# Optimization experiments

Hardware: AMD Instinct MI355X
Metric: run time of the kernel (lower is better)

## Reference

```python
import jax, jax.numpy as jnp
import numpy as np

HIDDEN = 2048
H = 16            # num heads
Q_RANK = 1536
KV_RANK = 512
D_NOPE = 128
D_ROPE = 64
D_QK = D_NOPE + D_ROPE   # 192
D_V = 128
ROPE_BASE = 10000.0
EPS = 1e-6


def _rms_norm(x, w):
    xf = x.astype(jnp.float32)
    var = jnp.mean(xf * xf, axis=-1, keepdims=True)
    return w * (xf * jax.lax.rsqrt(var + EPS)).astype(x.dtype)


def _rotate_half(x):
    x1, x2 = x[..., : x.shape[-1] // 2], x[..., x.shape[-1] // 2:]
    return jnp.concatenate((-x2, x1), axis=-1)


def _rope_cos_sin(position_ids, dtype):
    inv_freq = 1.0 / (ROPE_BASE ** (jnp.arange(0, D_ROPE, 2, dtype=jnp.float32) / D_ROPE))
    freqs = position_ids.astype(jnp.float32)[..., None] * inv_freq  # [b,s,32]
    emb = jnp.concatenate((freqs, freqs), axis=-1)                  # [b,s,64]
    return jnp.cos(emb).astype(dtype), jnp.sin(emb).astype(dtype)


def setup_inputs() -> dict:
    key = jax.random.key(0)
    ks = jax.random.split(key, 8)
    b, s = 1, 2048
    scale = 0.02
    return {
        "hidden_states": jax.random.normal(ks[0], (b, s, HIDDEN), jnp.float32),
        "position_ids": jnp.broadcast_to(jnp.arange(s, dtype=jnp.int64)[None, :], (b, s)),
        "q_a_w": jax.random.normal(ks[1], (Q_RANK, HIDDEN), jnp.float32) * scale,
        "q_a_ln_w": jnp.ones((Q_RANK,), jnp.float32),
        "q_b_w": jax.random.normal(ks[2], (H * D_QK, Q_RANK), jnp.float32) * scale,
        "kv_a_w": jax.random.normal(ks[3], (KV_RANK + D_ROPE, HIDDEN), jnp.float32) * scale,
        "kv_a_ln_w": jnp.ones((KV_RANK,), jnp.float32),
        "kv_b_w": jax.random.normal(ks[4], (H * (D_NOPE + D_V), KV_RANK), jnp.float32) * scale,
        "o_w": jax.random.normal(ks[5], (HIDDEN, H * D_V), jnp.float32) * scale,
    }


def reference(hidden_states, position_ids, q_a_w, q_a_ln_w, q_b_w, kv_a_w, kv_a_ln_w, kv_b_w, o_w):
    b, s, _ = hidden_states.shape
    softmax_scale = D_QK ** (-0.5)

    # Q path: low-rank down-proj -> RMSNorm -> up-proj
    q_a = hidden_states @ q_a_w.T                              # [b,s,q_rank]
    q = (_rms_norm(q_a, q_a_ln_w) @ q_b_w.T).reshape(b, s, H, D_QK)
    q_nope, q_pe = q[..., :D_NOPE], q[..., D_NOPE:]

    # KV path: joint down-proj -> split latent / rope part
    kv_a = hidden_states @ kv_a_w.T                            # [b,s,kv_rank+rope]
    compressed_kv = _rms_norm(kv_a[..., :KV_RANK], kv_a_ln_w)  # [b,s,kv_rank]
    k_pe = kv_a[..., KV_RANK:]                                 # [b,s,rope]
    kv_b = (compressed_kv @ kv_b_w.T).reshape(b, s, H, D_NOPE + D_V)
    k_nope, v = kv_b[..., :D_NOPE], kv_b[..., D_NOPE:]

    # decoupled RoPE on the rope slice
    cos, sin = _rope_cos_sin(position_ids, hidden_states.dtype)  # [b,s,64]
    cos, sin = cos[:, :, None, :], sin[:, :, None, :]            # [b,s,1,64]
    q_pe = q_pe * cos + _rotate_half(q_pe) * sin                 # [b,s,H,64]
    k_pe_h = jnp.broadcast_to(k_pe[:, :, None, :], (b, s, H, D_ROPE))
    k_pe_h = k_pe_h * cos + _rotate_half(k_pe_h) * sin

    q_full = jnp.concatenate([q_nope, q_pe], axis=-1)            # [b,s,H,192]
    k_full = jnp.concatenate([k_nope, k_pe_h], axis=-1)          # [b,s,H,192]

    # naive materialized attention (matches reference)
    scores = jnp.einsum("bqhd,bkhd->bhqk", q_full, k_full) * softmax_scale
    causal = jnp.triu(jnp.full((s, s), -jnp.inf, dtype=scores.dtype), k=1)
    scores = scores + causal
    probs = jax.nn.softmax(scores.astype(jnp.float32), axis=-1).astype(q_full.dtype)
    attn = jnp.einsum("bhqk,bkhd->bqhd", probs, v).reshape(b, s, H * D_V)
    return attn @ o_w.T
```

## Files before the change

kernel.cpp:

```cpp
#include <hip/hip_runtime.h>
#include <stdint.h>

#define S_LEN 2048
#define HIDDEN_ 2048
#define NH 16
#define QR 1536
#define KVR 512
#define DN 128
#define DR 64
#define DQK 192
#define DV 128
#define NQKV 2112

typedef __attribute__((ext_vector_type(8))) short bf16x8;
typedef __attribute__((ext_vector_type(4))) float f32x4;
typedef __attribute__((ext_vector_type(4))) unsigned short u16x4;
typedef unsigned short u16;
typedef unsigned int u32;

#define GLOAD_LDS16(g, l)                                                      \
    __builtin_amdgcn_global_load_lds(                                          \
        (const __attribute__((address_space(1))) void*)(g),                    \
        (__attribute__((address_space(3))) void*)(l), 16, 0, 0)

__device__ inline float bf2f(u16 x) {
    union { u32 u; float f; } v; v.u = ((u32)x) << 16; return v.f;
}
__device__ inline u16 f2bf(float f) {
    union { float f; u32 u; } v; v.f = f;
    u32 u = v.u;
    return (u16)((u + 0x7fffu + ((u >> 16) & 1u)) >> 16);
}

__global__ void cvt_multi(const float* s0, u16* d0, int n0,
                          const float* s1, u16* d1, int n1,
                          const float* s2, u16* d2, int n2,
                          const float* s3, u16* d3, int n3,
                          const float* s4, u16* d4, int n4,
                          const float* s5, u16* d5, int n5)
{
    const float* src; u16* dst; int n;
    switch (blockIdx.y) {
        case 0: src = s0; dst = d0; n = n0; break;
        case 1: src = s1; dst = d1; n = n1; break;
        case 2: src = s2; dst = d2; n = n2; break;
        case 3: src = s3; dst = d3; n = n3; break;
        case 4: src = s4; dst = d4; n = n4; break;
        default: src = s5; dst = d5; n = n5; break;
    }
    int i = (blockIdx.x * 256 + threadIdx.x) * 4;
    if (i + 3 < n) {
        float4 v = *(const float4*)(src + i);
        u16x4 o;
        o[0] = f2bf(v.x); o[1] = f2bf(v.y); o[2] = f2bf(v.z); o[3] = f2bf(v.w);
        *(u16x4*)(dst + i) = o;
    }
}

__device__ __forceinline__
void gemm_body(const u16* __restrict__ A, const u16* __restrict__ B,
               void* __restrict__ Cv, int M, int N, int Kloop, int ld,
               int out_f32, int bx, int by)
{
    __shared__ u16 sA[128 * 32];
    __shared__ u16 sB[128 * 32];
    const int tid  = threadIdx.x;
    const int wave = tid >> 6;
    const int lane = tid & 63;
    const int l16  = lane & 15;
    const int quad = lane >> 4;
    const int m_blk = by * 128;
    const int n_blk = bx * 128;
    const int wm = (wave >> 1) * 64;
    const int wn = (wave & 1) * 64;

    const f32x4 zero4 = {0.f, 0.f, 0.f, 0.f};
    f32x4 acc[4][4];
#pragma unroll
    for (int i = 0; i < 4; i++)
#pragma unroll
        for (int j = 0; j < 4; j++) acc[i][j] = zero4;

    const int srow = lane >> 2;
    const int scol = (lane & 3) * 8;

    for (int k0 = 0; k0 < Kloop; k0 += 32) {
        __syncthreads();
#pragma unroll
        for (int p = 0; p < 2; p++) {
            const int rbase = wave * 32 + p * 16;
            const int row = rbase + srow;
            const u16* ga = A + (size_t)(m_blk + row) * ld + k0 + scol;
            GLOAD_LDS16(ga, &sA[rbase * 32]);
            int brow = n_blk + row; if (brow >= N) brow = N - 1;
            const u16* gb = B + (size_t)brow * ld + k0 + scol;
            GLOAD_LDS16(gb, &sB[rbase * 32]);
        }
        __syncthreads();

        bf16x8 af[4], bfr[4];
#pragma unroll
        for (int i = 0; i < 4; i++)
            af[i] = *(const bf16x8*)(sA + (wm + i * 16 + l16) * 32 + quad * 8);
#pragma unroll
        for (int j = 0; j < 4; j++)
            bfr[j] = *(const bf16x8*)(sB + (wn + j * 16 + l16) * 32 + quad * 8);
#pragma unroll
        for (int i = 0; i < 4; i++)
#pragma unroll
            for (int j = 0; j < 4; j++)
                acc[i][j] = __builtin_amdgcn_mfma_f32_16x16x32_bf16(
                    af[i], bfr[j], acc[i][j], 0, 0, 0);
    }

#pragma unroll
    for (int i = 0; i < 4; i++)
#pragma unroll
        for (int j = 0; j < 4; j++)
#pragma unroll
            for (int r = 0; r < 4; r++) {
                int mrow = m_blk + wm + i * 16 + quad * 4 + r;
                int ncol = n_blk + wn + j * 16 + l16;
                if (ncol < N) {
                    if (out_f32)
                        ((float*)Cv)[(size_t)mrow * N + ncol] = acc[i][j][r];
                    else
                        ((u16*)Cv)[(size_t)mrow * N + ncol] = f2bf(acc[i][j][r]);
                }
            }
}

__global__ __launch_bounds__(256, 3)
void gemm_splitk(const u16* __restrict__ A, const u16* __restrict__ B,
                 float* __restrict__ C0, float* __restrict__ C1,
                 int M, int N, int Kh, int ld)
{
    float* C = blockIdx.z ? C1 : C0;
    gemm_body(A + (size_t)blockIdx.z * Kh, B + (size_t)blockIdx.z * Kh,
              C, M, N, Kh, ld, 1, blockIdx.x, blockIdx.y);
}

__global__ __launch_bounds__(256, 3)
void gemm_dual(const u16* A0, const u16* B0, u16* C0, int M0, int N0, int K0,
               const u16* A1, const u16* B1, u16* C1, int M1, int N1, int K1)
{
    if (blockIdx.z == 0) {
        if ((int)blockIdx.x >= (N0 + 127) / 128) return;
        gemm_body(A0, B0, C0, M0, N0, K0, K0, 0, blockIdx.x, blockIdx.y);
    } else {
        gemm_body(A1, B1, C1, M1, N1, K1, K1, 0, blockIdx.x, blockIdx.y);
    }
}

__global__ void rmsnorm2_k(const float* __restrict__ P0, const float* __restrict__ P1,
                           const float* __restrict__ W0, u16* __restrict__ Y0,
                           const float* __restrict__ W1, u16* __restrict__ Y1,
                           u16* __restrict__ kpe)
{
    const int row = blockIdx.x;
    const float* p0 = P0 + (size_t)row * NQKV;
    const float* p1 = P1 + (size_t)row * NQKV;
    __shared__ float xbuf[QR];
    __shared__ float red[4];
    int off, len; const float* W; u16* Y;
    if (blockIdx.y == 0) { off = 0;  len = QR;  W = W0; Y = Y0 + (size_t)row * QR;  }
    else                 { off = QR; len = KVR; W = W1; Y = Y1 + (size_t)row * KVR; }
    float ss = 0.f;
    for (int i = threadIdx.x; i < len; i += 256) {
        float v = p0[off + i] + p1[off + i];
        xbuf[i] = v;
        ss += v * v;
    }
#pragma unroll
    for (int o = 32; o; o >>= 1) ss += __shfl_down(ss, o, 64);
    if ((threadIdx.x & 63) == 0) red[threadIdx.x >> 6] = ss;
    __syncthreads();
    float tot = red[0] + red[1] + red[2] + red[3];
    float inv = 1.0f / sqrtf(tot / (float)len + 1e-6f);
    for (int i = threadIdx.x; i < len; i += 256)
        Y[i] = f2bf(W[i] * xbuf[i] * inv);
    if (blockIdx.y == 1 && threadIdx.x < DR) {
        int i = threadIdx.x;
        kpe[(size_t)row * DR + i] = f2bf(p0[QR + KVR + i] + p1[QR + KVR + i]);
    }
}

__global__ void rope_repack(const u16* __restrict__ q,
                            const u16* __restrict__ kvb,
                            const u16* __restrict__ kpe_b,
                            u16* __restrict__ Q, u16* __restrict__ Kf)
{
    const int s = blockIdx.x;
    const float pos = (float)s;
    const int t = threadIdx.x;
    __shared__ float cs[64], sn[64];
    __shared__ u16 kpe_r[64];
    if (t < 64) {
        int jf = t & 31;
        float freq = powf(10000.f, -(float)(2 * jf) / 64.f);
        float ang = pos * freq;
        cs[t] = cosf(ang);
        sn[t] = sinf(ang);
    }
    __syncthreads();
    if (t < 64) {
        int j = t;
        float x = bf2f(kpe_b[(size_t)s * DR + j]);
        float other = (j < 32) ? -bf2f(kpe_b[(size_t)s * DR + j + 32])
                               :  bf2f(kpe_b[(size_t)s * DR + j - 32]);
        kpe_r[j] = f2bf(x * cs[j] + other * sn[j]);
    }
    __syncthreads();

    for (int idx = t; idx < NH * DQK; idx += 256) {
        int h = idx / DQK, d = idx % DQK;
        const size_t qrow = (size_t)s * (NH * DQK) + h * DQK;
        u16 qv;
        if (d < DN) qv = q[qrow + d];
        else {
            int j = d - DN;
            float x = bf2f(q[qrow + DN + j]);
            float other = (j < 32) ? -bf2f(q[qrow + DN + j + 32])
                                   :  bf2f(q[qrow + DN + j - 32]);
            qv = f2bf(x * cs[j] + other * sn[j]);
        }
        Q[((size_t)h * S_LEN + s) * DQK + d] = qv;
        u16 kv;
        if (d < DN) kv = kvb[(size_t)s * (NH * 256) + h * 256 + d];
        else        kv = kpe_r[d - DN];
        Kf[((size_t)h * S_LEN + s) * DQK + d] = kv;
    }
}

__global__ void transpose_v(const u16* __restrict__ kvb, u16* __restrict__ Vt)
{
    __shared__ u16 tile[64][72];
    const int h  = blockIdx.z;
    const int s0 = blockIdx.x * 64;
    const int d0 = blockIdx.y * 64;
    const int t  = threadIdx.x;
#pragma unroll
    for (int p = 0; p < 2; p++) {
        int c = p * 256 + t;
        int r = c >> 3, col = (c & 7) * 8;
        *(bf16x8*)&tile[r][col] =
            *(const bf16x8*)&kvb[(size_t)(s0 + r) * (NH * 256) + h * 256 + 128 + d0 + col];
    }
    __syncthreads();
#pragma unroll
    for (int p = 0; p < 2; p++) {
        int c = p * 256 + t;
        int dr = c >> 3, sc = (c & 7) * 8;
        bf16x8 v;
#pragma unroll
        for (int j = 0; j < 8; j++) v[j] = (short)tile[sc + j][dr];
        *(bf16x8*)&Vt[((size_t)h * DV + d0 + dr) * S_LEN + s0 + sc] = v;
    }
}

__global__ __launch_bounds__(256, 3)
void mla_attn(const u16* __restrict__ Q, const u16* __restrict__ Kf,
              const u16* __restrict__ Vt, u16* __restrict__ attn,
              float* __restrict__ part)
{
    const int h  = blockIdx.y;
    const int bx = blockIdx.x;
    int s, tb, te, cIdx; bool direct;
    if (bx < 16)      { s = 16 + bx; tb = 0;  te = 32;        cIdx = 0; direct = false; }
    else if (bx < 32) { s = 47 - bx; tb = 32; te = 2 * s + 2; cIdx = 1; direct = false; }
    else              { s = 47 - bx; tb = 0;  te = 2 * s + 2; cIdx = 0; direct = true;  }

    const int wave  = threadIdx.x >> 6;
    const int lane  = threadIdx.x & 63;
    const int l16   = lane & 15;
    const int quad  = lane >> 4;
    const int q0    = s * 64 + wave * 16;
    const int qrow  = q0 + l16;

    const u16* Qh  = Q  + (size_t)h * S_LEN * DQK;
    const u16* Kh  = Kf + (size_t)h * S_LEN * DQK;
    const u16* Vth = Vt + (size_t)h * DV * S_LEN;

    __shared__ u16 sK[2][24 * 32 * 8];
    __shared__ u16 sV[2][4 * 128 * 8];
    __shared__ u16 pbuf[4][16][36];
    u16 (*pb)[36] = pbuf[wave];

    bf16x8 qf[6];
#pragma unroll
    for (int st = 0; st < 6; st++)
        qf[st] = *(const bf16x8*)(Qh + (size_t)qrow * DQK + st * 32 + quad * 8);

    const f32x4 zero4 = {0.f, 0.f, 0.f, 0.f};
    f32x4 oacc[8];
#pragma unroll
    for (int t = 0; t < 8; t++) oacc[t] = zero4;
    float mrow = -INFINITY, lrow = 0.f;

    const float scale = 0.07216878364870323f;

    auto stage = [&](int buf, int c0) {
#pragma unroll
        for (int g = 0; g < 3; g++) {
            int c = g * 256 + wave * 64 + lane;
            int row = c & 31, cg = c >> 5;
            GLOAD_LDS16(Kh + (size_t)(c0 + row) * DQK + cg * 8,
                        &sK[buf][(g * 256 + wave * 64) * 8]);
        }
#pragma unroll
        for (int g = 0; g < 2; g++) {
            int c = g * 256 + wave * 64 + lane;
            int d = c & 127, cg = c >> 7;
            GLOAD_LDS16(Vth + (size_t)d * S_LEN + c0 + cg * 8,
                        &sV[buf][(g * 256 + wave * 64) * 8]);
        }
    };

    stage(0, tb * 32);

    for (int kt = tb; kt < te; kt++) {
        const int c0  = kt * 32;
        const int cur = (kt - tb) & 1;
        __syncthreads();
        if (kt + 1 < te) stage(cur ^ 1, c0 + 32);

        if (c0 <= q0 + 15) {
            f32x4 s0 = zero4, s1 = zero4;
#pragma unroll
            for (int st = 0; st < 6; st++) {
                bf16x8 k0 = *(const bf16x8*)&sK[cur][((st * 4 + quad) * 32 + l16) * 8];
                bf16x8 k1 = *(const bf16x8*)&sK[cur][((st * 4 + quad) * 32 + 16 + l16) * 8];
                s0 = __builtin_amdgcn_mfma_f32_16x16x32_bf16(k0, qf[st], s0, 0, 0, 0);
                s1 = __builtin_amdgcn_mfma_f32_16x16x32_bf16(k1, qf[st], s1, 0, 0, 0);
            }
            bf16x8 vfr[8];
#pragma unroll
            for (int t = 0; t < 8; t++)
                vfr[t] = *(const bf16x8*)&sV[cur][(quad * 128 + t * 16 + l16) * 8];

            const bool full = (c0 + 31 <= q0);
            float v0[4], v1[4];
#pragma unroll
            for (int r = 0; r < 4; r++) {
                v0[r] = s0[r] * scale;
                v1[r] = s1[r] * scale;
                if (!full) {
                    if (c0 + quad * 4 + r > qrow)      v0[r] = -INFINITY;
                    if (c0 + 16 + quad * 4 + r > qrow) v1[r] = -INFINITY;
                }
            }
            float lm = fmaxf(fmaxf(fmaxf(v0[0], v0[1]), fmaxf(v0[2], v0[3])),
                             fmaxf(fmaxf(v1[0], v1[1]), fmaxf(v1[2], v1[3])));
            lm = fmaxf(lm, __shfl_xor(lm, 16, 64));
            lm = fmaxf(lm, __shfl_xor(lm, 32, 64));
            const float mnew  = fmaxf(mrow, lm);
            const float alpha = __expf(mrow - mnew);
            float p0[4], p1[4], rs = 0.f;
#pragma unroll
            for (int r = 0; r < 4; r++) {
                p0[r] = __expf(v0[r] - mnew);
                p1[r] = __expf(v1[r] - mnew);
                rs += p0[r] + p1[r];
            }
            rs += __shfl_xor(rs, 16, 64);
            rs += __shfl_xor(rs, 32, 64);
            lrow = lrow * alpha + rs;
            mrow = mnew;
#pragma unroll
            for (int t = 0; t < 8; t++) oacc[t] *= alpha;

            u16x4 pk0, pk1;
#pragma unroll
            for (int r = 0; r < 4; r++) { pk0[r] = f2bf(p0[r]); pk1[r] = f2bf(p1[r]); }
            *(u16x4*)&pb[l16][quad * 4]      = pk0;
            *(u16x4*)&pb[l16][16 + quad * 4] = pk1;
            asm volatile("s_waitcnt lgkmcnt(0)" ::: "memory");
            bf16x8 pfrag = *(const bf16x8*)(&pb[l16][quad * 8]);

#pragma unroll
            for (int t = 0; t < 8; t++)
                oacc[t] = __builtin_amdgcn_mfma_f32_16x16x32_bf16(vfr[t], pfrag,
                                                                  oacc[t], 0, 0, 0);
        }
    }

    if (direct) {
        const float linv = 1.0f / lrow;
#pragma unroll
        for (int t = 0; t < 8; t++) {
            u16x4 ov;
#pragma unroll
            for (int r = 0; r < 4; r++) ov[r] = f2bf(oacc[t][r] * linv);
            *(u16x4*)&attn[(size_t)qrow * (NH * DV) + h * DV + t * 16 + quad * 4] = ov;
        }
    } else {
        float* pout = part + ((size_t)(h * 16 + (s - 16)) * 2 + cIdx) * 8320;
        const int rowl = wave * 16 + l16;
#pragma unroll
        for (int t = 0; t < 8; t++) {
            float4 ov = {oacc[t][0], oacc[t][1], oacc[t][2], oacc[t][3]};
            *(float4*)&pout[(size_t)rowl * 128 + t * 16 + quad * 4] = ov;
        }
        if (quad == 0) {
            pout[8192 + rowl] = mrow;
            pout[8256 + rowl] = lrow;
        }
    }
}

__global__ void attn_combine(const float* __restrict__ part, u16* __restrict__ attn)
{
    const int h = blockIdx.y, sIdx = blockIdx.x;
    const int s = 16 + sIdx;
    const float* p0 = part + ((size_t)(h * 16 + sIdx) * 2 + 0) * 8320;
    const float* p1 = p0 + 8320;
    for (int e = threadIdx.x; e < 8192; e += 256) {
        int row = e >> 7, d = e & 127;
        float m0 = p0[8192 + row], m1 = p1[8192 + row];
        float l0 = p0[8256 + row], l1 = p1[8256 + row];
        float M  = fmaxf(m0, m1);
        float w0 = __expf(m0 - M), w1 = __expf(m1 - M);
        float o  = (w0 * p0[e] + w1 * p1[e]) / (w0 * l0 + w1 * l1);
        attn[(size_t)(s * 64 + row) * (NH * DV) + h * DV + d] = f2bf(o);
    }
}

__global__ void addf2(const float* __restrict__ a, const float* __restrict__ b,
                      float* __restrict__ o, int n)
{
    int i = (blockIdx.x * 256 + threadIdx.x) * 4;
    if (i + 3 < n) {
        float4 va = *(const float4*)(a + i);
        float4 vb = *(const float4*)(b + i);
        float4 vo = {va.x + vb.x, va.y + vb.y, va.z + vb.z, va.w + vb.w};
        *(float4*)(o + i) = vo;
    }
}

extern "C" void kernel_launch(void* const* d_in, const int* in_sizes, int n_in,
                              void* d_out, int out_size, void* d_ws, size_t ws_size,
                              hipStream_t stream)
{
    const float* hid      = (const float*)d_in[0];
    const float* q_a_w    = (const float*)d_in[2];
    const float* q_a_ln_w = (const float*)d_in[3];
    const float* q_b_w    = (const float*)d_in[4];
    const float* kv_a_w   = (const float*)d_in[5];
    const float* kv_a_ln_w= (const float*)d_in[6];
    const float* kv_b_w   = (const float*)d_in[7];
    const float* o_w      = (const float*)d_in[8];

    char* base = (char*)d_ws;
    u16* qkvaw_b = (u16*)(base + 0);
    u16* qbw_b   = (u16*)(base + 8650752);
    u16* kvbw_b  = (u16*)(base + 18087936);
    u16* ow_b    = (u16*)(base + 22282240);
    u16* hid_b   = (u16*)(base + 30670848);
    float* P0    = (float*)(base + 39059456);
    float* P1    = (float*)(base + 56360960);
    u16* q_n     = (u16*)(base + 73662464);
    u16* ckv     = (u16*)(base + 79953920);
    u16* kpe_b   = (u16*)(base + 82051072);
    u16* qb      = (u16*)(base + 82313216);
    u16* kvb     = (u16*)(base + 94896128);
    u16* Qb      = (u16*)(base + 39059456);
    u16* Kb      = (u16*)(base + 51642368);
    u16* Vtb     = (u16*)(base + 64225280);
    u16* attnb   = (u16*)(base + 72613888);
    float* partb = (float*)(base + 94896128);
    float* PO0   = (float*)(base + 82313216);
    float* PO1   = (float*)(base + 99090432);

    cvt_multi<<<dim3(4608, 6), 256, 0, stream>>>(
        hid,    hid_b,                          HIDDEN_ * S_LEN,
        q_a_w,  qkvaw_b,                        QR * HIDDEN_,
        kv_a_w, qkvaw_b + (size_t)QR * HIDDEN_, (KVR + DR) * HIDDEN_,
        q_b_w,  qbw_b,                          NH * DQK * QR,
        kv_b_w, kvbw_b,                         NH * 256 * KVR,
        o_w,    ow_b,                           HIDDEN_ * NH * DV);

    gemm_splitk<<<dim3((NQKV + 127) / 128, S_LEN / 128, 2), 256, 0, stream>>>(
        hid_b, qkvaw_b, P0, P1, S_LEN, NQKV, HIDDEN_ / 2, HIDDEN_);
    rmsnorm2_k<<<dim3(S_LEN, 2), 256, 0, stream>>>(
        P0, P1, q_a_ln_w, q_n, kv_a_ln_w, ckv, kpe_b);
    gemm_dual<<<dim3(32, S_LEN / 128, 2), 256, 0, stream>>>(
        q_n, qbw_b, qb,  S_LEN, NH * DQK, QR,
        ckv, kvbw_b, kvb, S_LEN, NH * 256, KVR);
    rope_repack<<<S_LEN, 256, 0, stream>>>(qb, kvb, kpe_b, Qb, Kb);
    transpose_v<<<dim3(S_LEN / 64, DV / 64, NH), 256, 0, stream>>>(kvb, Vtb);
    mla_attn<<<dim3(48, NH), 256, 0, stream>>>(Qb, Kb, Vtb, attnb, partb);
    attn_combine<<<dim3(16, NH), 256, 0, stream>>>(partb, attnb);
    gemm_splitk<<<dim3(HIDDEN_ / 128, S_LEN / 128, 2), 256, 0, stream>>>(
        attnb, ow_b, PO0, PO1, S_LEN, HIDDEN_, HIDDEN_ / 2, HIDDEN_);
    addf2<<<dim3((S_LEN * HIDDEN_) / 1024), 256, 0, stream>>>(
        PO0, PO1, (float*)d_out, S_LEN * HIDDEN_);
}
```

Measured before the change: 351.7 us.

## Pre-tile K and V into contiguous per-tile LDS image layout

The producer kernels now write K and transposed V in a blocked layout where each 32-key tile is one contiguous chunk that matches the shared-memory arrangement exactly. The attention kernel's async global-to-LDS loads then read consecutive 16-byte chunks instead of strided rows, which should improve coalescing. The Q/K prep loop is also vectorized to 8-element stores. Any other consumer of Kf/Vt has to use the new layout.

```diff
diff --git a/kernel.cpp b/kernel.cpp
--- a/kernel.cpp
+++ b/kernel.cpp
@@ -11,6 +11,9 @@
 #define DQK 192
 #define DV 128
 #define NQKV 2112
+
+#define KT_STRIDE 6144
+#define VT_STRIDE 4096
 
 typedef __attribute__((ext_vector_type(8))) short bf16x8;
 typedef __attribute__((ext_vector_type(4))) float f32x4;
@@ -212,23 +215,31 @@
     }
     __syncthreads();
 
-    for (int idx = t; idx < NH * DQK; idx += 256) {
-        int h = idx / DQK, d = idx % DQK;
-        const size_t qrow = (size_t)s * (NH * DQK) + h * DQK;
-        u16 qv;
-        if (d < DN) qv = q[qrow + d];
-        else {
-            int j = d - DN;
-            float x = bf2f(q[qrow + DN + j]);
-            float other = (j < 32) ? -bf2f(q[qrow + DN + j + 32])
-                                   :  bf2f(q[qrow + DN + j - 32]);
-            qv = f2bf(x * cs[j] + other * sn[j]);
+    for (int idx = t; idx < NH * 24; idx += 256) {
+        const int h  = idx / 24;
+        const int cg = idx % 24;
+        const int d0v = cg * 8;
+        const size_t qbase = (size_t)s * (NH * DQK) + h * DQK;
+        bf16x8 qv, kv;
+        if (d0v < DN) {
+            qv = *(const bf16x8*)(q + qbase + d0v);
+            kv = *(const bf16x8*)(kvb + (size_t)s * (NH * 256) + h * 256 + d0v);
+        } else {
+            const int j0 = d0v - DN;
+#pragma unroll
+            for (int e = 0; e < 8; e++) {
+                int j = j0 + e;
+                float x = bf2f(q[qbase + DN + j]);
+                float other = (j < 32) ? -bf2f(q[qbase + DN + j + 32])
+                                       :  bf2f(q[qbase + DN + j - 32]);
+                qv[e] = (short)f2bf(x * cs[j] + other * sn[j]);
+                kv[e] = (short)kpe_r[j];
+            }
         }
-        Q[((size_t)h * S_LEN + s) * DQK + d] = qv;
-        u16 kv;
-        if (d < DN) kv = kvb[(size_t)s * (NH * 256) + h * 256 + d];
-        else        kv = kpe_r[d - DN];
-        Kf[((size_t)h * S_LEN + s) * DQK + d] = kv;
+        *(bf16x8*)&Q[((size_t)h * S_LEN + s) * DQK + d0v] = qv;
+        const size_t koff = (size_t)(h * 64 + (s >> 5)) * KT_STRIDE
+                          + (size_t)(cg * 32 + (s & 31)) * 8;
+        *(bf16x8*)&Kf[koff] = kv;
     }
 }
 
@@ -254,7 +265,12 @@
         bf16x8 v;
 #pragma unroll
         for (int j = 0; j < 8; j++) v[j] = (short)tile[sc + j][dr];
-        *(bf16x8*)&Vt[((size_t)h * DV + d0 + dr) * S_LEN + s0 + sc] = v;
+        const int s_abs   = s0 + sc;
+        const int kt      = s_abs >> 5;
+        const int schunk  = (s_abs & 31) >> 3;
+        const size_t voff = (size_t)(h * 64 + kt) * VT_STRIDE
+                          + (size_t)(schunk * 128 + (d0 + dr)) * 8;
+        *(bf16x8*)&Vt[voff] = v;
     }
 }
 
@@ -278,8 +294,8 @@
     const int qrow  = q0 + l16;
 
     const u16* Qh  = Q  + (size_t)h * S_LEN * DQK;
-    const u16* Kh  = Kf + (size_t)h * S_LEN * DQK;
-    const u16* Vth = Vt + (size_t)h * DV * S_LEN;
+    const u16* Kh  = Kf + (size_t)h * 64 * KT_STRIDE;
+    const u16* Vth = Vt + (size_t)h * 64 * VT_STRIDE;
 
     __shared__ u16 sK[2][24 * 32 * 8];
     __shared__ u16 sV[2][4 * 128 * 8];
@@ -299,30 +315,26 @@
 
     const float scale = 0.07216878364870323f;
 
-    auto stage = [&](int buf, int c0) {
-#pragma unroll
-        for (int g = 0; g < 3; g++) {
-            int c = g * 256 + wave * 64 + lane;
-            int row = c & 31, cg = c >> 5;
-            GLOAD_LDS16(Kh + (size_t)(c0 + row) * DQK + cg * 8,
+    auto stage = [&](int buf, int kt) {
+        const u16* kp = Kh + (size_t)kt * KT_STRIDE;
+#pragma unroll
+        for (int g = 0; g < 3; g++)
+            GLOAD_LDS16(kp + (g * 256 + wave * 64 + lane) * 8,
                         &sK[buf][(g * 256 + wave * 64) * 8]);
-        }
-#pragma unroll
-        for (int g = 0; g < 2; g++) {
-            int c = g * 256 + wave * 64 + lane;
-            int d = c & 127, cg = c >> 7;
-            GLOAD_LDS16(Vth + (size_t)d * S_LEN + c0 + cg * 8,
+        const u16* vp = Vth + (size_t)kt * VT_STRIDE;
+#pragma unroll
+        for (int g = 0; g < 2; g++)
+            GLOAD_LDS16(vp + (g * 256 + wave * 64 + lane) * 8,
                         &sV[buf][(g * 256 + wave * 64) * 8]);
-        }
     };
 
-    stage(0, tb * 32);
+    stage(0, tb);
 
     for (int kt = tb; kt < te; kt++) {
         const int c0  = kt * 32;
         const int cur = (kt - tb) & 1;
         __syncthreads();
-        if (kt + 1 < te) stage(cur ^ 1, c0 + 32);
+        if (kt + 1 < te) stage(cur ^ 1, kt + 1);
 
         if (c0 <= q0 + 15) {
             f32x4 s0 = zero4, s1 = zero4;
```

Result: no change. 350.0 us (-0.5%).
